# Kernel tuning notes

Measured on AMD Instinct MI355X. Metric: run time of the kernel, lower is better.

Reference implementation:

```python
import jax, jax.numpy as jnp
import numpy as np

B, N, C, H = 8, 2048, 384, 6
D = C // H  # head dim = 64
SCALE = D ** -0.5


def setup_inputs() -> dict:
    key = jax.random.key(0)
    k1, k2, k3, k4 = jax.random.split(key, 4)
    x = jax.random.normal(k1, (B, N, C), dtype=jnp.float32)
    prompt = jnp.zeros((1,), dtype=jnp.float32)  # unused by forward
    mask = jax.random.uniform(k2, (B, N, N), dtype=jnp.float32)
    qkv_w = jax.random.normal(k3, (3 * C, C), dtype=jnp.float32) * (C ** -0.5)
    proj_w = jax.random.normal(k4, (C, C), dtype=jnp.float32) * (C ** -0.5)
    proj_b = jnp.zeros((C,), dtype=jnp.float32)
    return {"x": x, "prompt": prompt, "mask": mask,
            "qkv_w": qkv_w, "proj_w": proj_w, "proj_b": proj_b}


def reference(x, prompt, mask, qkv_w, proj_w, proj_b):
    b, n, c = x.shape
    # qkv: Linear(dim, 3*dim, bias=False) -> (B,N,3,H,D) -> (3,B,H,N,D)
    qkv = (x @ qkv_w.T).reshape(b, n, 3, H, D).transpose(2, 0, 3, 1, 4)
    q, k, v = qkv[0], qkv[1], qkv[2]
    # attn scores with additive mask (mask * -1e5), softmax over keys
    attn = jnp.einsum('bhqd,bhkd->bhqk', q, k) * SCALE
    attn = attn + (mask * -100000.0)[:, None, :, :]
    attn = jax.nn.softmax(attn, axis=-1)
    out = jnp.einsum('bhqk,bhkd->bhqd', attn, v)  # (B,H,N,D)
    out = out.transpose(0, 2, 1, 3).reshape(b, n, c)
    return out @ proj_w.T + proj_b
```

## Files before the change

kernel.cpp:

```cpp
#include <hip/hip_runtime.h>
#include <stdint.h>
#include <math.h>

#define BB 8
#define SEQ 2048
#define CDIM 384
#define NH 6
#define HD 64
#define QKVN 1152

typedef __attribute__((ext_vector_type(8))) __bf16 bf16x8;
typedef __attribute__((ext_vector_type(4))) float f32x4;
typedef __attribute__((ext_vector_type(4))) unsigned short ushort4v;

__device__ __forceinline__ unsigned short f2bf(float f) {
  unsigned int u = __float_as_uint(f);
  u += 0x7fffu + ((u >> 16) & 1u);
  return (unsigned short)(u >> 16);
}

__global__ void k_convert(const float* __restrict__ src, unsigned short* __restrict__ dst, int n4) {
  int i = blockIdx.x * blockDim.x + threadIdx.x;
  if (i >= n4) return;
  float4 f = reinterpret_cast<const float4*>(src)[i];
  ushort4v u;
  u.x = f2bf(f.x); u.y = f2bf(f.y); u.z = f2bf(f.z); u.w = f2bf(f.w);
  reinterpret_cast<ushort4v*>(dst)[i] = u;
}

__device__ __forceinline__ void gload_lds16(const unsigned short* g, unsigned short* l) {
  __builtin_amdgcn_global_load_lds((const __attribute__((address_space(1))) void*)g,
                                   (__attribute__((address_space(3))) void*)l, 16, 0, 0);
}

template<int OUT_F32>
__global__ __launch_bounds__(256, 2) void k_gemm_bt(
    const unsigned short* __restrict__ A, const unsigned short* __restrict__ Bm,
    unsigned short* __restrict__ Cb, float* __restrict__ Cf,
    const float* __restrict__ bias, int M, int Nc, int K)
{
  __shared__ unsigned short lA[128 * 32];
  __shared__ unsigned short lB[128 * 32];
  const int t = threadIdx.x;
  const int w = t >> 6, l = t & 63;
  const int wr = w >> 1, wc = w & 1;
  const int row0 = blockIdx.x * 128, col0 = blockIdx.y * 128;
  const f32x4 vzero = {0.f, 0.f, 0.f, 0.f};
  f32x4 acc[4][4];
#pragma unroll
  for (int m = 0; m < 4; ++m)
#pragma unroll
    for (int n = 0; n < 4; ++n) acc[m][n] = vzero;

  const int srow = w * 16 + (l >> 2);
  const int scol = (l & 3) * 8;
  const int lr = l & 15, kc = (l >> 4) * 8;

  for (int k0 = 0; k0 < K; k0 += 32) {
#pragma unroll
    for (int r = 0; r < 2; ++r) {
      gload_lds16(A + (size_t)(row0 + r * 64 + srow) * K + k0 + scol,
                  &lA[(r * 64 + srow) * 32 + scol]);
      gload_lds16(Bm + (size_t)(col0 + r * 64 + srow) * K + k0 + scol,
                  &lB[(r * 64 + srow) * 32 + scol]);
    }
    __syncthreads();
    bf16x8 af[4], bfr[4];
#pragma unroll
    for (int m = 0; m < 4; ++m)
      af[m] = *(const bf16x8*)&lA[(wr * 64 + m * 16 + lr) * 32 + kc];
#pragma unroll
    for (int n = 0; n < 4; ++n)
      bfr[n] = *(const bf16x8*)&lB[(wc * 64 + n * 16 + lr) * 32 + kc];
#pragma unroll
    for (int m = 0; m < 4; ++m)
#pragma unroll
      for (int n = 0; n < 4; ++n)
        acc[m][n] = __builtin_amdgcn_mfma_f32_16x16x32_bf16(af[m], bfr[n], acc[m][n], 0, 0, 0);
    __syncthreads();
  }

#pragma unroll
  for (int m = 0; m < 4; ++m) {
    const int row = row0 + wr * 64 + m * 16 + (l >> 4) * 4;
#pragma unroll
    for (int n = 0; n < 4; ++n) {
      const int col = col0 + wc * 64 + n * 16 + (l & 15);
      if (OUT_F32) {
        const float bv = bias[col];
#pragma unroll
        for (int j = 0; j < 4; ++j)
          Cf[(size_t)(row + j) * Nc + col] = acc[m][n][j] + bv;
      } else {
#pragma unroll
        for (int j = 0; j < 4; ++j)
          Cb[(size_t)(row + j) * Nc + col] = f2bf(acc[m][n][j]);
      }
    }
  }
}

__global__ void k_vtrans(const unsigned short* __restrict__ qkv, unsigned short* __restrict__ vt)
{
  __shared__ unsigned short tile[64][76];
  const int bh = blockIdx.x;
  const int b = bh / NH, h = bh - b * NH;
  const int n0 = blockIdx.y * 64;
  const int t = threadIdx.x;
  const int rr0 = t >> 4;
  const int c4 = (t & 15) * 4;
  const unsigned short* src = qkv + (size_t)(b * SEQ + n0) * QKVN + 2 * CDIM + h * HD;
#pragma unroll
  for (int rr = 0; rr < 4; ++rr) {
    int n = rr * 16 + rr0;
    ushort4v v = *(const ushort4v*)(src + (size_t)n * QKVN + c4);
    *(ushort4v*)&tile[n][c4] = v;
  }
  __syncthreads();
  unsigned short* dst = vt + (size_t)bh * HD * SEQ + n0;
#pragma unroll
  for (int rr = 0; rr < 4; ++rr) {
    int d = rr * 16 + rr0;
    ushort4v v;
    v.x = tile[c4 + 0][d];
    v.y = tile[c4 + 1][d];
    v.z = tile[c4 + 2][d];
    v.w = tile[c4 + 3][d];
    *(ushort4v*)(dst + (size_t)d * SEQ + c4) = v;
  }
}

__global__ __launch_bounds__(512, 4) void k_attn(
    const unsigned short* __restrict__ qkv, const float* __restrict__ mask,
    const unsigned short* __restrict__ vt, unsigned short* __restrict__ aout)
{
  const int bid = blockIdx.x;
  const int b = bid & 7;
  const int g2 = bid >> 3;
  const int h = g2 % NH;
  const int nt = g2 / NH;
  const int t = threadIdx.x;
  const int w = t >> 6, l = t & 63;
  const int gk = l >> 4, c = l & 15;
  const int q0 = nt * 128 + w * 16;

  __shared__ unsigned short lK[2][4096];
  __shared__ unsigned short lV[2][4096];
  __shared__ __bf16 lP[8][16 * 80];
  __bf16* pw = lP[w];

  const unsigned short* qb = qkv + (size_t)(b * SEQ + q0) * QKVN + h * HD;
  const unsigned short* kb = qkv + (size_t)(b * SEQ) * QKVN + CDIM + h * HD;
  const unsigned short* vb = vt + (size_t)(b * NH + h) * HD * SEQ;
  const float* mrow = mask + ((size_t)b * SEQ + q0) * SEQ;

  const int trow = t >> 3, tg = t & 7;
  const int glog = tg ^ (trow & 7);
  const size_t kSrc = (size_t)trow * QKVN + glog * 8;
  const size_t vSrc = (size_t)trow * SEQ + glog * 8;
  const int tid8 = t * 8;

  const int fr0 = c * 64 + ((gk) ^ (c & 7)) * 8;
  const int fr1 = c * 64 + ((4 + gk) ^ (c & 7)) * 8;

  bf16x8 qf0 = *(const bf16x8*)(qb + (size_t)c * QKVN + gk * 8);
  bf16x8 qf1 = *(const bf16x8*)(qb + (size_t)c * QKVN + 32 + gk * 8);
#pragma unroll
  for (int i = 0; i < 8; ++i) {
    qf0[i] = (__bf16)((float)qf0[i] * 0.18033688f);
    qf1[i] = (__bf16)((float)qf1[i] * 0.18033688f);
  }

  const __bf16 one = (__bf16)1.0f;
  const bf16x8 vones = {one, one, one, one, one, one, one, one};
  const f32x4 vzero = {0.f, 0.f, 0.f, 0.f};
  f32x4 acco[4];
  f32x4 asum = vzero;
  float mreg[4];
#pragma unroll
  for (int r = 0; r < 4; ++r) mreg[r] = -INFINITY;
#pragma unroll
  for (int dt = 0; dt < 4; ++dt) acco[dt] = vzero;

  gload_lds16(kb + kSrc, &lK[0][tid8]);
  gload_lds16(vb + vSrc, &lV[0][tid8]);
  float mk[4][4];
#pragma unroll
  for (int j = 0; j < 4; ++j)
#pragma unroll
    for (int r = 0; r < 4; ++r)
      mk[j][r] = mrow[(size_t)(4 * gk + r) * SEQ + 16 * j + c];
  int buf = 0;

  for (int kt = 0; kt < SEQ; kt += 64) {
    const bool haveNext = (kt + 64 < SEQ);
    __syncthreads();
    if (haveNext) {
      gload_lds16(kb + (size_t)(kt + 64) * QKVN + kSrc, &lK[buf ^ 1][tid8]);
      gload_lds16(vb + (kt + 64) + vSrc, &lV[buf ^ 1][tid8]);
    }

    f32x4 s[4];
#pragma unroll
    for (int j = 0; j < 4; ++j) {
      bf16x8 kfa = *(const bf16x8*)&lK[buf][j * 1024 + fr0];
      bf16x8 kfb = *(const bf16x8*)&lK[buf][j * 1024 + fr1];
      s[j] = __builtin_amdgcn_mfma_f32_16x16x32_bf16(qf0, kfa, vzero, 0, 0, 0);
      s[j] = __builtin_amdgcn_mfma_f32_16x16x32_bf16(qf1, kfb, s[j], 0, 0, 0);
    }

    float mk2[4][4];
    if (haveNext) {
#pragma unroll
      for (int j = 0; j < 4; ++j)
#pragma unroll
        for (int r = 0; r < 4; ++r)
          mk2[j][r] = mrow[(size_t)(4 * gk + r) * SEQ + kt + 64 + 16 * j + c];
    }

    float tm[4];
#pragma unroll
    for (int j = 0; j < 4; ++j)
#pragma unroll
      for (int r = 0; r < 4; ++r)
        s[j][r] = fmaf(mk[j][r], -144269.50f, s[j][r]);
#pragma unroll
    for (int r = 0; r < 4; ++r)
      tm[r] = fmaxf(fmaxf(fmaxf(s[0][r], s[1][r]), s[2][r]), s[3][r]);
#pragma unroll
    for (int off = 1; off < 16; off <<= 1)
#pragma unroll
      for (int r = 0; r < 4; ++r)
        tm[r] = fmaxf(tm[r], __shfl_xor(tm[r], off));

    bool nd = (tm[0] > mreg[0] + 8.f) || (tm[1] > mreg[1] + 8.f) ||
              (tm[2] > mreg[2] + 8.f) || (tm[3] > mreg[3] + 8.f);
    if (__any(nd)) {
#pragma unroll
      for (int r = 0; r < 4; ++r) {
        const float mn = fmaxf(mreg[r], tm[r]);
        const float al = __builtin_amdgcn_exp2f(mreg[r] - mn);
        mreg[r] = mn;
        asum[r] *= al;
#pragma unroll
        for (int dt = 0; dt < 4; ++dt) acco[dt][r] *= al;
      }
    }

    __asm__ volatile("" ::: "memory");
#pragma unroll
    for (int j = 0; j < 4; ++j)
#pragma unroll
      for (int r = 0; r < 4; ++r)
        pw[(4 * gk + r) * 80 + 16 * j + c] = (__bf16)__builtin_amdgcn_exp2f(s[j][r] - mreg[r]);
    __asm__ volatile("" ::: "memory");
    bf16x8 pf0 = *(const bf16x8*)&pw[c * 80 + gk * 8];
    bf16x8 pf1 = *(const bf16x8*)&pw[c * 80 + 32 + gk * 8];

#pragma unroll
    for (int dt = 0; dt < 4; ++dt) {
      bf16x8 vf0 = *(const bf16x8*)&lV[buf][dt * 1024 + fr0];
      bf16x8 vf1 = *(const bf16x8*)&lV[buf][dt * 1024 + fr1];
      acco[dt] = __builtin_amdgcn_mfma_f32_16x16x32_bf16(pf0, vf0, acco[dt], 0, 0, 0);
      acco[dt] = __builtin_amdgcn_mfma_f32_16x16x32_bf16(pf1, vf1, acco[dt], 0, 0, 0);
    }
    asum = __builtin_amdgcn_mfma_f32_16x16x32_bf16(pf0, vones, asum, 0, 0, 0);
    asum = __builtin_amdgcn_mfma_f32_16x16x32_bf16(pf1, vones, asum, 0, 0, 0);

    if (haveNext) {
#pragma unroll
      for (int j = 0; j < 4; ++j)
#pragma unroll
        for (int r = 0; r < 4; ++r)
          mk[j][r] = mk2[j][r];
    }
    buf ^= 1;
  }

  unsigned short* ob = aout + (size_t)(b * SEQ + q0) * CDIM + h * HD;
#pragma unroll
  for (int r = 0; r < 4; ++r) {
    const float inv = 1.0f / asum[r];
#pragma unroll
    for (int dt = 0; dt < 4; ++dt)
      ob[(size_t)(4 * gk + r) * CDIM + dt * 16 + c] = f2bf(acco[dt][r] * inv);
  }
}

extern "C" void kernel_launch(void* const* d_in, const int* in_sizes, int n_in,
                              void* d_out, int out_size, void* d_ws, size_t ws_size,
                              hipStream_t stream) {
  (void)in_sizes; (void)n_in; (void)out_size; (void)ws_size;
  const float* x      = (const float*)d_in[0];
  const float* mask   = (const float*)d_in[2];
  const float* qkv_w  = (const float*)d_in[3];
  const float* proj_w = (const float*)d_in[4];
  const float* proj_b = (const float*)d_in[5];
  float* out = (float*)d_out;
  char* ws = (char*)d_ws;

  unsigned short* xb    = (unsigned short*)(ws + 0);
  unsigned short* wqb   = (unsigned short*)(ws + 12582912);
  unsigned short* wpb   = (unsigned short*)(ws + 13467648);
  unsigned short* qkvb  = (unsigned short*)(ws + 13762560);
  unsigned short* vtb   = (unsigned short*)(ws + 51511296);
  unsigned short* aoutb = (unsigned short*)(ws + 64094208);

  k_convert<<<6144, 256, 0, stream>>>(x, xb, 1572864);
  k_convert<<<432, 256, 0, stream>>>(qkv_w, wqb, 110592);
  k_convert<<<144, 256, 0, stream>>>(proj_w, wpb, 36864);
  k_gemm_bt<0><<<dim3(128, 9), 256, 0, stream>>>(xb, wqb, qkvb, nullptr, nullptr, 16384, 1152, 384);
  k_vtrans<<<dim3(48, 32), 256, 0, stream>>>(qkvb, vtb);
  k_attn<<<768, 512, 0, stream>>>(qkvb, mask, vtb, aoutb);
  k_gemm_bt<1><<<dim3(128, 3), 256, 0, stream>>>(aoutb, wpb, nullptr, out, proj_b, 16384, 384, 384);
}
```

Before: 193.5 us.

## Transpose QK^T MFMA so each lane owns a query row; halve attention block size

The QK^T MFMA operands are swapped so that S comes out transposed. Each lane then holds one query row's scores, which lets it load the mask as contiguous float4s and do the row max and row sum with two cross-lane shuffles instead of four. Row sums are now accumulated in registers rather than through extra MFMAs against a ones vector. P is packed to bf16 with v_cvt_pk_bf16_f32 and written to a swizzled 32-bit LDS buffer. Blocks shrink from 512 to 256 threads (1536 blocks, 64 queries each), which doubles how often K/V tiles are reloaded per query row in exchange for more, smaller blocks.

```diff
diff --git a/kernel.cpp b/kernel.cpp
--- a/kernel.cpp
+++ b/kernel.cpp
@@ -130,7 +130,7 @@
   }
 }
 
-__global__ __launch_bounds__(512, 4) void k_attn(
+__global__ __launch_bounds__(256, 4) void k_attn(
     const unsigned short* __restrict__ qkv, const float* __restrict__ mask,
     const unsigned short* __restrict__ vt, unsigned short* __restrict__ aout)
 {
@@ -142,26 +142,26 @@
   const int t = threadIdx.x;
   const int w = t >> 6, l = t & 63;
   const int gk = l >> 4, c = l & 15;
-  const int q0 = nt * 128 + w * 16;
+  const int q0 = nt * 64 + w * 16;
 
   __shared__ unsigned short lK[2][4096];
   __shared__ unsigned short lV[2][4096];
-  __shared__ __bf16 lP[8][16 * 80];
-  __bf16* pw = lP[w];
+  __shared__ unsigned int lP[4][512];
+  unsigned int* prow = lP[w] + c * 32;
 
   const unsigned short* qb = qkv + (size_t)(b * SEQ + q0) * QKVN + h * HD;
   const unsigned short* kb = qkv + (size_t)(b * SEQ) * QKVN + CDIM + h * HD;
   const unsigned short* vb = vt + (size_t)(b * NH + h) * HD * SEQ;
-  const float* mrow = mask + ((size_t)b * SEQ + q0) * SEQ;
+  const float* mrowc = mask + ((size_t)b * SEQ + q0 + c) * SEQ;
 
   const int trow = t >> 3, tg = t & 7;
   const int glog = tg ^ (trow & 7);
   const size_t kSrc = (size_t)trow * QKVN + glog * 8;
   const size_t vSrc = (size_t)trow * SEQ + glog * 8;
-  const int tid8 = t * 8;
 
   const int fr0 = c * 64 + ((gk) ^ (c & 7)) * 8;
   const int fr1 = c * 64 + ((4 + gk) ^ (c & 7)) * 8;
+  const int cx = (c & 7) << 2;
 
   bf16x8 qf0 = *(const bf16x8*)(qb + (size_t)c * QKVN + gk * 8);
   bf16x8 qf1 = *(const bf16x8*)(qb + (size_t)c * QKVN + 32 + gk * 8);
@@ -171,33 +171,32 @@
     qf1[i] = (__bf16)((float)qf1[i] * 0.18033688f);
   }
 
-  const __bf16 one = (__bf16)1.0f;
-  const bf16x8 vones = {one, one, one, one, one, one, one, one};
   const f32x4 vzero = {0.f, 0.f, 0.f, 0.f};
   f32x4 acco[4];
-  f32x4 asum = vzero;
-  float mreg[4];
-#pragma unroll
-  for (int r = 0; r < 4; ++r) mreg[r] = -INFINITY;
+  float mreg = -INFINITY, asum = 0.f;
 #pragma unroll
   for (int dt = 0; dt < 4; ++dt) acco[dt] = vzero;
 
-  gload_lds16(kb + kSrc, &lK[0][tid8]);
-  gload_lds16(vb + vSrc, &lV[0][tid8]);
-  float mk[4][4];
+#pragma unroll
+  for (int j = 0; j < 2; ++j) {
+    gload_lds16(kb + (size_t)j * 32 * QKVN + kSrc, &lK[0][j * 2048 + t * 8]);
+    gload_lds16(vb + (size_t)j * 32 * SEQ + vSrc, &lV[0][j * 2048 + t * 8]);
+  }
+  float4 mk[4];
 #pragma unroll
   for (int j = 0; j < 4; ++j)
-#pragma unroll
-    for (int r = 0; r < 4; ++r)
-      mk[j][r] = mrow[(size_t)(4 * gk + r) * SEQ + 16 * j + c];
+    mk[j] = *(const float4*)(mrowc + 16 * j + 4 * gk);
   int buf = 0;
 
   for (int kt = 0; kt < SEQ; kt += 64) {
     const bool haveNext = (kt + 64 < SEQ);
     __syncthreads();
     if (haveNext) {
-      gload_lds16(kb + (size_t)(kt + 64) * QKVN + kSrc, &lK[buf ^ 1][tid8]);
-      gload_lds16(vb + (kt + 64) + vSrc, &lV[buf ^ 1][tid8]);
+#pragma unroll
+      for (int j = 0; j < 2; ++j) {
+        gload_lds16(kb + (size_t)(kt + 64 + j * 32) * QKVN + kSrc, &lK[buf ^ 1][j * 2048 + t * 8]);
+        gload_lds16(vb + (kt + 64) + (size_t)j * 32 * SEQ + vSrc, &lV[buf ^ 1][j * 2048 + t * 8]);
+      }
     }
 
     f32x4 s[4];
@@ -205,57 +204,76 @@
     for (int j = 0; j < 4; ++j) {
       bf16x8 kfa = *(const bf16x8*)&lK[buf][j * 1024 + fr0];
       bf16x8 kfb = *(const bf16x8*)&lK[buf][j * 1024 + fr1];
-      s[j] = __builtin_amdgcn_mfma_f32_16x16x32_bf16(qf0, kfa, vzero, 0, 0, 0);
-      s[j] = __builtin_amdgcn_mfma_f32_16x16x32_bf16(qf1, kfb, s[j], 0, 0, 0);
-    }
-
-    float mk2[4][4];
+      s[j] = __builtin_amdgcn_mfma_f32_16x16x32_bf16(kfa, qf0, vzero, 0, 0, 0);
+      s[j] = __builtin_amdgcn_mfma_f32_16x16x32_bf16(kfb, qf1, s[j], 0, 0, 0);
+    }
+
+#pragma unroll
+    for (int j = 0; j < 4; ++j) {
+      const float* mkf = (const float*)&mk[j];
+#pragma unroll
+      for (int r = 0; r < 4; ++r)
+        s[j][r] = fmaf(mkf[r], -144269.50f, s[j][r]);
+    }
+
     if (haveNext) {
 #pragma unroll
       for (int j = 0; j < 4; ++j)
+        mk[j] = *(const float4*)(mrowc + kt + 64 + 16 * j + 4 * gk);
+    }
+
+    float tm = fmaxf(fmaxf(fmaxf(s[0][0], s[0][1]), fmaxf(s[0][2], s[0][3])),
+                     fmaxf(fmaxf(s[1][0], s[1][1]), fmaxf(s[1][2], s[1][3])));
+    tm = fmaxf(tm, fmaxf(fmaxf(fmaxf(s[2][0], s[2][1]), fmaxf(s[2][2], s[2][3])),
+                         fmaxf(fmaxf(s[3][0], s[3][1]), fmaxf(s[3][2], s[3][3]))));
+    tm = fmaxf(tm, __shfl_xor(tm, 16));
+    tm = fmaxf(tm, __shfl_xor(tm, 32));
+
+    if (__any(tm > mreg + 8.f)) {
+      const float mn = fmaxf(mreg, tm);
+      const float al = __builtin_amdgcn_exp2f(mreg - mn);
+      mreg = mn;
+      asum *= al;
+      float alr[4];
+#pragma unroll
+      for (int r = 0; r < 4; ++r)
+        alr[r] = __shfl(al, 20 * gk + r);
+#pragma unroll
+      for (int dt = 0; dt < 4; ++dt)
 #pragma unroll
         for (int r = 0; r < 4; ++r)
-          mk2[j][r] = mrow[(size_t)(4 * gk + r) * SEQ + kt + 64 + 16 * j + c];
-    }
-
-    float tm[4];
+          acco[dt][r] *= alr[r];
+    }
+
 #pragma unroll
     for (int j = 0; j < 4; ++j)
 #pragma unroll
       for (int r = 0; r < 4; ++r)
-        s[j][r] = fmaf(mk[j][r], -144269.50f, s[j][r]);
-#pragma unroll
-    for (int r = 0; r < 4; ++r)
-      tm[r] = fmaxf(fmaxf(fmaxf(s[0][r], s[1][r]), s[2][r]), s[3][r]);
-#pragma unroll
-    for (int off = 1; off < 16; off <<= 1)
-#pragma unroll
-      for (int r = 0; r < 4; ++r)
-        tm[r] = fmaxf(tm[r], __shfl_xor(tm[r], off));
-
-    bool nd = (tm[0] > mreg[0] + 8.f) || (tm[1] > mreg[1] + 8.f) ||
-              (tm[2] > mreg[2] + 8.f) || (tm[3] > mreg[3] + 8.f);
-    if (__any(nd)) {
-#pragma unroll
-      for (int r = 0; r < 4; ++r) {
-        const float mn = fmaxf(mreg[r], tm[r]);
-        const float al = __builtin_amdgcn_exp2f(mreg[r] - mn);
-        mreg[r] = mn;
-        asum[r] *= al;
-#pragma unroll
-        for (int dt = 0; dt < 4; ++dt) acco[dt][r] *= al;
-      }
-    }
-
+        s[j][r] = __builtin_amdgcn_exp2f(s[j][r] - mreg);
+    float rs = ((s[0][0] + s[0][1]) + (s[0][2] + s[0][3]))
+             + ((s[1][0] + s[1][1]) + (s[1][2] + s[1][3]))
+             + ((s[2][0] + s[2][1]) + (s[2][2] + s[2][3]))
+             + ((s[3][0] + s[3][1]) + (s[3][2] + s[3][3]));
+    rs += __shfl_xor(rs, 16);
+    rs += __shfl_xor(rs, 32);
+    asum += rs;
+
+    unsigned int pk[8];
+#pragma unroll
+    for (int j = 0; j < 4; ++j) {
+      asm("v_cvt_pk_bf16_f32 %0, %1, %2" : "=v"(pk[2 * j]) : "v"(s[j][0]), "v"(s[j][1]));
+      asm("v_cvt_pk_bf16_f32 %0, %1, %2" : "=v"(pk[2 * j + 1]) : "v"(s[j][2]), "v"(s[j][3]));
+    }
     __asm__ volatile("" ::: "memory");
 #pragma unroll
-    for (int j = 0; j < 4; ++j)
-#pragma unroll
-      for (int r = 0; r < 4; ++r)
-        pw[(4 * gk + r) * 80 + 16 * j + c] = (__bf16)__builtin_amdgcn_exp2f(s[j][r] - mreg[r]);
+    for (int j = 0; j < 4; ++j) {
+      prow[(8 * j + 2 * gk + 0) ^ cx] = pk[2 * j];
+      prow[(8 * j + 2 * gk + 1) ^ cx] = pk[2 * j + 1];
+    }
     __asm__ volatile("" ::: "memory");
-    bf16x8 pf0 = *(const bf16x8*)&pw[c * 80 + gk * 8];
-    bf16x8 pf1 = *(const bf16x8*)&pw[c * 80 + 32 + gk * 8];
+    bf16x8 pf0 = *(const bf16x8*)(prow + ((4 * gk) ^ cx));
+    bf16x8 pf1 = *(const bf16x8*)(prow + ((16 + 4 * gk) ^ cx));
+    __asm__ volatile("" ::: "memory");
 
 #pragma unroll
     for (int dt = 0; dt < 4; ++dt) {
@@ -264,27 +282,19 @@
       acco[dt] = __builtin_amdgcn_mfma_f32_16x16x32_bf16(pf0, vf0, acco[dt], 0, 0, 0);
       acco[dt] = __builtin_amdgcn_mfma_f32_16x16x32_bf16(pf1, vf1, acco[dt], 0, 0, 0);
     }
-    asum = __builtin_amdgcn_mfma_f32_16x16x32_bf16(pf0, vones, asum, 0, 0, 0);
-    asum = __builtin_amdgcn_mfma_f32_16x16x32_bf16(pf1, vones, asum, 0, 0, 0);
-
-    if (haveNext) {
-#pragma unroll
-      for (int j = 0; j < 4; ++j)
-#pragma unroll
-        for (int r = 0; r < 4; ++r)
-          mk[j][r] = mk2[j][r];
-    }
     buf ^= 1;
   }
 
+  float invr[4];
+#pragma unroll
+  for (int r = 0; r < 4; ++r)
+    invr[r] = 1.0f / __shfl(asum, 20 * gk + r);
   unsigned short* ob = aout + (size_t)(b * SEQ + q0) * CDIM + h * HD;
 #pragma unroll
-  for (int r = 0; r < 4; ++r) {
-    const float inv = 1.0f / asum[r];
+  for (int r = 0; r < 4; ++r)
 #pragma unroll
     for (int dt = 0; dt < 4; ++dt)
-      ob[(size_t)(4 * gk + r) * CDIM + dt * 16 + c] = f2bf(acco[dt][r] * inv);
-  }
+      ob[(size_t)(4 * gk + r) * CDIM + dt * 16 + c] = f2bf(acco[dt][r] * invr[r]);
 }
 
 extern "C" void kernel_launch(void* const* d_in, const int* in_sizes, int n_in,
@@ -311,6 +321,6 @@
   k_convert<<<144, 256, 0, stream>>>(proj_w, wpb, 36864);
   k_gemm_bt<0><<<dim3(128, 9), 256, 0, stream>>>(xb, wqb, qkvb, nullptr, nullptr, 16384, 1152, 384);
   k_vtrans<<<dim3(48, 32), 256, 0, stream>>>(qkvb, vtb);
-  k_attn<<<768, 512, 0, stream>>>(qkvb, mask, vtb, aoutb);
+  k_attn<<<1536, 256, 0, stream>>>(qkvb, mask, vtb, aoutb);
   k_gemm_bt<1><<<dim3(128, 3), 256, 0, stream>>>(aoutb, wpb, nullptr, out, proj_b, 16384, 384, 384);
 }
```

After: 191.1 us. No clear change (-1.2%).
